# Kernel optimization log

Measured on AMD Instinct MI355X. Metric: run time of the kernel, lower is better.

The kernel has to match this reference:

```python
import jax, jax.numpy as jnp
import numpy as np

DIM = 1024
HID = 2048
E = 8
K = 2
INV_SQRT2 = 1.0 / 1.41421356237


def setup_inputs() -> dict:
    key = jax.random.key(0)
    ks = jax.random.split(key, 10)
    s = lambda fan_in: 1.0 / np.sqrt(fan_in)
    return {
        "x": jax.random.normal(ks[0], (4, 2048, DIM), dtype=jnp.float32),
        "gate_w": jax.random.uniform(ks[1], (DIM, E), jnp.float32, -s(DIM), s(DIM)),
        "gate_b": jnp.zeros((E,), jnp.float32),
        "w1": jax.random.uniform(ks[2], (E, DIM, HID), jnp.float32, -s(DIM), s(DIM)),
        "b1": jnp.zeros((E, HID), jnp.float32),
        "w2": jax.random.uniform(ks[3], (E, DIM, HID), jnp.float32, -s(DIM), s(DIM)),
        "b2": jnp.zeros((E, HID), jnp.float32),
        "w3": jax.random.uniform(ks[4], (E, HID, DIM), jnp.float32, -s(HID), s(HID)),
        "b3": jnp.zeros((E, DIM), jnp.float32),
    }


def reference(x, gate_w, gate_b, w1, b1, w2, b2, w3, b3):
    # Gating
    logits = jnp.einsum("bsd,de->bse", x, gate_w) + gate_b          # [b,s,E]
    scores = jax.nn.softmax(logits, axis=-1)
    topk_scores, topk_idx = jax.lax.top_k(scores, K)                  # [b,s,K]

    # Load-balance (entropy) loss over mean expert usage
    usage = scores.mean(axis=(0, 1))                                   # [E]
    lb_loss = -(usage * jnp.log(usage + 1e-9)).sum()

    # Per-token combine weight for each expert: score if expert in top-k else 0
    onehot = jax.nn.one_hot(topk_idx, E, dtype=x.dtype)               # [b,s,K,E]
    comb = (topk_scores[..., None] * onehot).sum(axis=2)              # [b,s,E]

    # SwiGLU experts (batched over E via einsum)
    h = jnp.einsum("bsd,edh->ebsh", x, w1) + b1[:, None, None, :]
    g = jax.nn.silu(jnp.einsum("bsd,edh->ebsh", x, w2) + b2[:, None, None, :])
    eo = jnp.einsum("ebsh,ehd->ebsd", h * g, w3) + b3[:, None, None, :]
    eo = eo * INV_SQRT2

    # Weighted combine (zero weight where expert not selected)
    out = jnp.einsum("ebsd,bse->bsd", eo, comb)
    return out, lb_loss
```

## Files before the change

kernel.cpp:

```cpp
#include <hip/hip_runtime.h>
#include <cstdio>

#define NTOK 8192
#define DIM 1024
#define HID 2048
#define NE 8
#define NPAIR (NTOK * 2)

typedef __attribute__((ext_vector_type(8))) short bf16x8;
typedef __attribute__((ext_vector_type(4))) float f32x4;

typedef const __attribute__((address_space(1))) void* gas_ptr;
typedef __attribute__((address_space(3))) void* las_ptr;

__device__ __forceinline__ void async16(const void* g, void* s) {
  __builtin_amdgcn_global_load_lds((gas_ptr)g, (las_ptr)s, 16, 0, 0);
}

__device__ __forceinline__ unsigned short f2bf(float f) {
  unsigned int u = __float_as_uint(f);
  u = (u + 0x7fff + ((u >> 16) & 1)) >> 16;
  return (unsigned short)u;
}

__device__ __forceinline__ float bf2f(unsigned short u) {
  return __uint_as_float((unsigned int)u << 16);
}


#define S_BARRIER __builtin_amdgcn_s_barrier()
#define VM_WAIT(N) asm volatile("s_waitcnt vmcnt(" #N ")" ::: "memory")
#define LGKM0 asm volatile("s_waitcnt lgkmcnt(0)" ::: "memory")
#define CFENCE asm volatile("" ::: "memory")

__global__ __launch_bounds__(256) void prepgate_kernel(
    const float* __restrict__ w1, const float* __restrict__ w2,
    const float* __restrict__ w3, unsigned short* __restrict__ w1bt,
    unsigned short* __restrict__ w2bt, unsigned short* __restrict__ w3bt,
    const float* __restrict__ x, const float* __restrict__ gw,
    const float* __restrict__ gb, unsigned short* __restrict__ xb,
    float* __restrict__ scores, int* __restrict__ route_e,
    float* __restrict__ route_w) {
  __shared__ float smem[NE * DIM];
  const int bx = blockIdx.x;
  const int tid = threadIdx.x;

  if (bx < 12288) {
    float (*tT)[65] = reinterpret_cast<float(*)[65]>(smem);
    const int z = bx >> 9;
    const int bxx = bx & 511;
    const int m = z >> 3, e = z & 7;
    int R, C;
    const float* in;
    unsigned short* outp;
    if (m == 0)      { R = DIM; C = HID; in = w1; outp = w1bt; }
    else if (m == 1) { R = DIM; C = HID; in = w2; outp = w2bt; }
    else             { R = HID; C = DIM; in = w3; outp = w3bt; }
    in += (size_t)e * DIM * HID;
    outp += (size_t)e * DIM * HID;

    const int tilesx = C >> 6;
    const int c0 = (bxx % tilesx) * 64;
    const int r0 = (bxx / tilesx) * 64;

    const int cq = tid & 15;
    const int rr = tid >> 4;
#pragma unroll
    for (int p = 0; p < 4; p++) {
      const int r = rr + p * 16;
      const float4 v = *(const float4*)(in + (size_t)(r0 + r) * C + c0 + cq * 4);
      tT[cq * 4 + 0][r] = v.x;
      tT[cq * 4 + 1][r] = v.y;
      tT[cq * 4 + 2][r] = v.z;
      tT[cq * 4 + 3][r] = v.w;
    }
    __syncthreads();
    const int cc8 = tid & 7;
    const int rr2 = tid >> 3;
#pragma unroll
    for (int p = 0; p < 2; p++) {
      const int cc = rr2 + p * 32;
      bf16x8 o;
#pragma unroll
      for (int k = 0; k < 8; k++) o[k] = (short)f2bf(tT[cc][cc8 * 8 + k]);
      *(bf16x8*)(outp + (size_t)(c0 + cc) * R + r0 + cc8 * 8) = o;
    }
    return;
  }

  float (*sgwT)[DIM] = reinterpret_cast<float(*)[DIM]>(smem);
  const int g = bx - 12288;
#pragma unroll
  for (int i = 0; i < 8; i++) {
    const int j = i * 256 + tid;
    const float4 v = ((const float4*)gw)[j];
    const int d = j >> 1, e0 = (j & 1) * 4;
    sgwT[e0 + 0][d] = v.x; sgwT[e0 + 1][d] = v.y;
    sgwT[e0 + 2][d] = v.z; sgwT[e0 + 3][d] = v.w;
  }
  __syncthreads();

  const int wv = tid >> 6, lane = tid & 63;
  const int t = g * 4 + wv;
  float acc[NE] = {0.f, 0.f, 0.f, 0.f, 0.f, 0.f, 0.f, 0.f};
  const float4* x4 = (const float4*)(x + (size_t)t * DIM);
#pragma unroll
  for (int i = 0; i < 4; i++) {
    const float4 xv = x4[i * 64 + lane];
    const int d4 = i * 64 + lane;
    ushort4 xbv;
    xbv.x = f2bf(xv.x); xbv.y = f2bf(xv.y);
    xbv.z = f2bf(xv.z); xbv.w = f2bf(xv.w);
    *(ushort4*)(xb + (size_t)t * DIM + d4 * 4) = xbv;
#pragma unroll
    for (int e = 0; e < NE; e++) {
      const float4 wv4 = *(const float4*)&sgwT[e][d4 * 4];
      acc[e] += xv.x * wv4.x + xv.y * wv4.y + xv.z * wv4.z + xv.w * wv4.w;
    }
  }
#pragma unroll
  for (int e = 0; e < NE; e++)
#pragma unroll
    for (int s = 32; s; s >>= 1) acc[e] += __shfl_xor(acc[e], s, 64);

  if (lane == 0) {
    float l[NE], m = -1e30f;
#pragma unroll
    for (int e = 0; e < NE; e++) { l[e] = acc[e] + gb[e]; m = fmaxf(m, l[e]); }
    float p[NE], sum = 0.f;
#pragma unroll
    for (int e = 0; e < NE; e++) { p[e] = __expf(l[e] - m); sum += p[e]; }
    const float inv = 1.f / sum;
    float s[NE];
#pragma unroll
    for (int e = 0; e < NE; e++) { s[e] = p[e] * inv; scores[t * NE + e] = s[e]; }
    int i1 = 0;
    for (int e = 1; e < NE; e++) if (s[e] > s[i1]) i1 = e;
    int i2 = -1;
    for (int e = 0; e < NE; e++) {
      if (e == i1) continue;
      if (i2 < 0 || s[e] > s[i2]) i2 = e;
    }
    route_e[t * 2] = i1; route_e[t * 2 + 1] = i2;
    route_w[t * 2] = s[i1]; route_w[t * 2 + 1] = s[i2];
  }
}

__global__ void finalize_kernel(const float* __restrict__ scores,
                                const int* __restrict__ route_e,
                                int* __restrict__ ctrl,
                                float* __restrict__ out_lb) {
  __shared__ float red[1024];
  __shared__ int hist[NE];
  const int tid = threadIdx.x;
  if (tid < NE) hist[tid] = 0;
  const int e = tid & 7, row = tid >> 3;
  float s = 0.f;
  for (int i = 0; i < 64; i++) s += scores[(size_t)(row + i * 128) * NE + e];
  red[tid] = s;
  __syncthreads();
#pragma unroll
  for (int i = 0; i < 16; i++)
    atomicAdd(&hist[route_e[i * 1024 + tid]], 1);
  for (int st = 512; st >= 8; st >>= 1) {
    __syncthreads();
    if (tid < st) red[tid] += red[tid + st];
  }
  __syncthreads();
  if (tid == 0) {
    float lb = 0.f;
    for (int ee = 0; ee < NE; ee++) {
      const float u = red[ee] * (1.f / 8192.f);
      lb -= u * __logf(u + 1e-9f);
    }
    *out_lb = lb;
    int o = 0;
    for (int ee = 0; ee < NE; ee++) {
      ctrl[ee] = hist[ee];
      ctrl[8 + ee] = o;
      ctrl[17 + ee] = o;
      o += hist[ee];
    }
    ctrl[16] = o;
  }
}

__global__ __launch_bounds__(256) void scatter_kernel(
    const int* __restrict__ route_e, const float* __restrict__ route_w,
    int* __restrict__ ctrl, int* __restrict__ tok_list,
    float* __restrict__ pair_w, int* __restrict__ pair_pos) {
  __shared__ int lh[NE];
  __shared__ int lbase[NE];
  const int tid = threadIdx.x;
  const int t = blockIdx.x * 256 + tid;
  if (tid < NE) lh[tid] = 0;
  __syncthreads();
  const int e0 = route_e[t * 2], e1 = route_e[t * 2 + 1];
  const int p0 = atomicAdd(&lh[e0], 1);
  const int p1 = atomicAdd(&lh[e1], 1);
  __syncthreads();
  if (tid < NE) lbase[tid] = atomicAdd(&ctrl[17 + tid], lh[tid]);
  __syncthreads();
  const int q0 = lbase[e0] + p0;
  const int q1 = lbase[e1] + p1;
  tok_list[q0] = t;
  pair_w[q0] = route_w[t * 2] * 0.70710678118654752f;
  pair_pos[t * 2] = q0;
  tok_list[q1] = t;
  pair_w[q1] = route_w[t * 2 + 1] * 0.70710678118654752f;
  pair_pos[t * 2 + 1] = q1;
}

__global__ __launch_bounds__(512) void stage1_kernel(
    const unsigned short* __restrict__ xb, const unsigned short* __restrict__ w1bt,
    const unsigned short* __restrict__ w2bt, const float* __restrict__ b1,
    const float* __restrict__ b2, const int* __restrict__ tok_list,
    const int* __restrict__ ctrl, unsigned short* __restrict__ act) {
  const int hbid = blockIdx.x;
  const int xcd = hbid & 7, j = hbid >> 3;
  const int unit = xcd + 8 * (j >> 4);
  const int e = unit >> 5;
  const int ytile = unit & 31;
  const int h0 = (j & 15) * 128;

  const int cnt = ctrl[e];
  if (ytile * 256 >= cnt) return;
  const int off = ctrl[8 + e];
  const int rows = min(256, cnt - ytile * 256);

  __shared__ unsigned short sX[4][256 * 32];
  __shared__ unsigned short sW1[4][128 * 32];
  __shared__ unsigned short sW2[4][128 * 32];

  const int tid = threadIdx.x;
  const int wv = tid >> 6, lane = tid & 63;
  const int cl = ((tid & 3) ^ ((tid >> 3) & 3)) * 8;

  const unsigned short* w1p = w1bt + (size_t)e * HID * DIM + (size_t)h0 * DIM;
  const unsigned short* w2p = w2bt + (size_t)e * HID * DIM + (size_t)h0 * DIM;
  const unsigned short* gx0 =
      xb + (size_t)tok_list[off + ytile * 256 + min(tid >> 2, rows - 1)] * DIM + cl;
  const unsigned short* gx1 =
      xb + (size_t)tok_list[off + ytile * 256 + min(128 + (tid >> 2), rows - 1)] * DIM + cl;
  const unsigned short* gw1 = w1p + (size_t)(tid >> 2) * DIM + cl;
  const unsigned short* gw2 = w2p + (size_t)(tid >> 2) * DIM + cl;

  f32x4 ah[8][2], ag[8][2];
#pragma unroll
  for (int i = 0; i < 8; i++)
#pragma unroll
    for (int j2 = 0; j2 < 2; j2++) {
      ah[i][j2] = (f32x4){0.f, 0.f, 0.f, 0.f};
      ag[i][j2] = (f32x4){0.f, 0.f, 0.f, 0.f};
    }

  const int wr = wv >> 2, wc = wv & 3;
  const int l15 = lane & 15, q = lane >> 4;
  const int pch = (q ^ ((l15 >> 1) & 3)) * 8;

#define S1_STAGE(B)                                   \
  do {                                                \
    async16(gx0, sX[B] + (wv * 64) * 8);              \
    async16(gx1, sX[B] + (512 + wv * 64) * 8);        \
    async16(gw1, sW1[B] + (wv * 64) * 8);             \
    async16(gw2, sW2[B] + (wv * 64) * 8);             \
    gx0 += 32; gx1 += 32; gw1 += 32; gw2 += 32;       \
  } while (0)

  S1_STAGE(0); S1_STAGE(1); S1_STAGE(2);
  VM_WAIT(8);
  S_BARRIER;
  CFENCE;

  const int NT = DIM / 32;
  for (int t = 0; t < NT; t++) {
    const int cur = t & 3;
    bf16x8 bx[8], a1[2], a2[2];
    {
      const unsigned short* xs = sX[cur];
      const unsigned short* w1s = sW1[cur];
      const unsigned short* w2s = sW2[cur];
#pragma unroll
      for (int j2 = 0; j2 < 2; j2++) {
        a1[j2] = *(const bf16x8*)(w1s + (wc * 32 + j2 * 16 + l15) * 32 + pch);
        a2[j2] = *(const bf16x8*)(w2s + (wc * 32 + j2 * 16 + l15) * 32 + pch);
      }
#pragma unroll
      for (int i = 0; i < 8; i++)
        bx[i] = *(const bf16x8*)(xs + (wr * 128 + i * 16 + l15) * 32 + pch);
    }
    if (t < NT - 3) {
      const int nb = (t + 3) & 3;
      S1_STAGE(nb);
    }
    __builtin_amdgcn_s_setprio(1);
#pragma unroll
    for (int i = 0; i < 8; i++) {
      ah[i][0] = __builtin_amdgcn_mfma_f32_16x16x32_bf16(a1[0], bx[i], ah[i][0], 0, 0, 0);
      ag[i][0] = __builtin_amdgcn_mfma_f32_16x16x32_bf16(a2[0], bx[i], ag[i][0], 0, 0, 0);
      ah[i][1] = __builtin_amdgcn_mfma_f32_16x16x32_bf16(a1[1], bx[i], ah[i][1], 0, 0, 0);
      ag[i][1] = __builtin_amdgcn_mfma_f32_16x16x32_bf16(a2[1], bx[i], ag[i][1], 0, 0, 0);
    }
    __builtin_amdgcn_s_setprio(0);
    LGKM0;
    __builtin_amdgcn_sched_barrier(0);
    if (t < NT - 3) VM_WAIT(8);
    else if (t == NT - 3) VM_WAIT(4);
    else if (t == NT - 2) VM_WAIT(0);
    CFENCE;
    S_BARRIER;
  }
#undef S1_STAGE

  f32x4 b1v[2], b2v[2];
#pragma unroll
  for (int j2 = 0; j2 < 2; j2++) {
    const int hc = h0 + wc * 32 + j2 * 16 + q * 4;
    b1v[j2] = *(const f32x4*)(b1 + e * HID + hc);
    b2v[j2] = *(const f32x4*)(b2 + e * HID + hc);
  }
#pragma unroll
  for (int i = 0; i < 8; i++) {
    const int trow = wr * 128 + i * 16 + l15;
    if (trow < rows) {
      const size_t gp = (size_t)(off + ytile * 256 + trow) * HID;
#pragma unroll
      for (int j2 = 0; j2 < 2; j2++) {
        const int hc = h0 + wc * 32 + j2 * 16 + q * 4;
        ushort4 o;
        {
          const float hh = ah[i][j2][0] + b1v[j2][0];
          const float gg = ag[i][j2][0] + b2v[j2][0];
          o.x = f2bf(hh * (gg / (1.f + __expf(-gg))));
        }
        {
          const float hh = ah[i][j2][1] + b1v[j2][1];
          const float gg = ag[i][j2][1] + b2v[j2][1];
          o.y = f2bf(hh * (gg / (1.f + __expf(-gg))));
        }
        {
          const float hh = ah[i][j2][2] + b1v[j2][2];
          const float gg = ag[i][j2][2] + b2v[j2][2];
          o.z = f2bf(hh * (gg / (1.f + __expf(-gg))));
        }
        {
          const float hh = ah[i][j2][3] + b1v[j2][3];
          const float gg = ag[i][j2][3] + b2v[j2][3];
          o.w = f2bf(hh * (gg / (1.f + __expf(-gg))));
        }
        *(ushort4*)(act + gp + hc) = o;
      }
    }
  }
}

__global__ __launch_bounds__(512) void stage2s_kernel(
    const unsigned short* __restrict__ act, const unsigned short* __restrict__ w3bt,
    const float* __restrict__ b3, const float* __restrict__ pair_w,
    const int* __restrict__ ctrl, unsigned short* __restrict__ pair_out) {
  const int hbid = blockIdx.x;
  const int xcd = hbid & 7, j = hbid >> 3;
  const int unit = xcd + 8 * (j >> 2);
  const int e = unit >> 5;
  const int ytile = unit & 31;
  const int d0 = (j & 3) * 256;

  const int cnt = ctrl[e];
  if (ytile * 256 >= cnt) return;
  const int off = ctrl[8 + e];
  const int rows = min(256, cnt - ytile * 256);
  const int rbase = off + ytile * 256;

  __shared__ unsigned short sA[4][256 * 32];
  __shared__ unsigned short sW[4][256 * 32];

  const int tid = threadIdx.x;
  const int wv = tid >> 6, lane = tid & 63;
  const int cl = ((tid & 3) ^ ((tid >> 3) & 3)) * 8;

  const unsigned short* w3p = w3bt + (size_t)e * DIM * HID + (size_t)d0 * HID;
  const unsigned short* ga0 =
      act + (size_t)(rbase + min(tid >> 2, rows - 1)) * HID + cl;
  const unsigned short* ga1 =
      act + (size_t)(rbase + min(128 + (tid >> 2), rows - 1)) * HID + cl;
  const unsigned short* gw0 = w3p + (size_t)(tid >> 2) * HID + cl;
  const unsigned short* gw1 = w3p + (size_t)(128 + (tid >> 2)) * HID + cl;

  f32x4 acc[8][4];
#pragma unroll
  for (int i = 0; i < 8; i++)
#pragma unroll
    for (int jj = 0; jj < 4; jj++) acc[i][jj] = (f32x4){0.f, 0.f, 0.f, 0.f};

  const int wr = wv >> 2, wc = wv & 3;
  const int l15 = lane & 15, q = lane >> 4;
  const int pch = (q ^ ((l15 >> 1) & 3)) * 8;

#define S2_STAGE(B)                                   \
  do {                                                \
    async16(ga0, sA[B] + (wv * 64) * 8);              \
    async16(ga1, sA[B] + (512 + wv * 64) * 8);        \
    async16(gw0, sW[B] + (wv * 64) * 8);              \
    async16(gw1, sW[B] + (512 + wv * 64) * 8);        \
    ga0 += 32; ga1 += 32; gw0 += 32; gw1 += 32;       \
  } while (0)

  S2_STAGE(0); S2_STAGE(1); S2_STAGE(2);
  VM_WAIT(8);
  S_BARRIER;
  CFENCE;

  const int NT = HID / 32;
  for (int t = 0; t < NT; t++) {
    const int cur = t & 3;
    bf16x8 af[8], bf[4];
    {
      const unsigned short* as = sA[cur];
      const unsigned short* ws = sW[cur];
#pragma unroll
      for (int jj = 0; jj < 4; jj++)
        bf[jj] = *(const bf16x8*)(ws + (wc * 64 + jj * 16 + l15) * 32 + pch);
#pragma unroll
      for (int i = 0; i < 8; i++)
        af[i] = *(const bf16x8*)(as + (wr * 128 + i * 16 + l15) * 32 + pch);
    }
    if (t < NT - 3) {
      const int nb = (t + 3) & 3;
      S2_STAGE(nb);
    }
    __builtin_amdgcn_s_setprio(1);
#pragma unroll
    for (int i = 0; i < 8; i++)
#pragma unroll
      for (int jj = 0; jj < 4; jj++)
        acc[i][jj] =
            __builtin_amdgcn_mfma_f32_16x16x32_bf16(af[i], bf[jj], acc[i][jj], 0, 0, 0);
    __builtin_amdgcn_s_setprio(0);
    LGKM0;
    __builtin_amdgcn_sched_barrier(0);
    if (t < NT - 3) VM_WAIT(8);
    else if (t == NT - 3) VM_WAIT(4);
    else if (t == NT - 2) VM_WAIT(0);
    CFENCE;
    S_BARRIER;
  }
#undef S2_STAGE

#pragma unroll
  for (int i = 0; i < 8; i++)
#pragma unroll
    for (int rg = 0; rg < 4; rg++) {
      const int row = wr * 128 + i * 16 + q * 4 + rg;
      if (row < rows) {
        const int pr = rbase + row;
        const float wt = pair_w[pr];
#pragma unroll
        for (int jj = 0; jj < 4; jj++) {
          const int dcol = d0 + wc * 64 + jj * 16 + l15;
          pair_out[(size_t)pr * DIM + dcol] = f2bf((acc[i][jj][rg] + b3[e * DIM + dcol]) * wt);
        }
      }
    }
}

__global__ __launch_bounds__(512) void stage2a_kernel(
    const unsigned short* __restrict__ act, const unsigned short* __restrict__ w3bt,
    const float* __restrict__ b3, const int* __restrict__ tok_list,
    const float* __restrict__ pair_w, const int* __restrict__ ctrl,
    float* __restrict__ out) {
  const int hbid = blockIdx.x;
  const int xcd = hbid & 7, j = hbid >> 3;
  const int unit = xcd + 8 * (j >> 2);
  const int e = unit >> 5;
  const int ytile = unit & 31;
  const int d0 = (j & 3) * 256;

  const int cnt = ctrl[e];
  if (ytile * 256 >= cnt) return;
  const int off = ctrl[8 + e];
  const int rows = min(256, cnt - ytile * 256);
  const int rbase = off + ytile * 256;

  __shared__ unsigned short sA[4][256 * 32];
  __shared__ unsigned short sW[4][256 * 32];

  const int tid = threadIdx.x;
  const int wv = tid >> 6, lane = tid & 63;
  const int cl = ((tid & 3) ^ ((tid >> 3) & 3)) * 8;

  const unsigned short* w3p = w3bt + (size_t)e * DIM * HID + (size_t)d0 * HID;
  const unsigned short* ga0 =
      act + (size_t)(rbase + min(tid >> 2, rows - 1)) * HID + cl;
  const unsigned short* ga1 =
      act + (size_t)(rbase + min(128 + (tid >> 2), rows - 1)) * HID + cl;
  const unsigned short* gw0 = w3p + (size_t)(tid >> 2) * HID + cl;
  const unsigned short* gw1 = w3p + (size_t)(128 + (tid >> 2)) * HID + cl;

  f32x4 acc[8][4];
#pragma unroll
  for (int i = 0; i < 8; i++)
#pragma unroll
    for (int jj = 0; jj < 4; jj++) acc[i][jj] = (f32x4){0.f, 0.f, 0.f, 0.f};

  const int wr = wv >> 2, wc = wv & 3;
  const int l15 = lane & 15, q = lane >> 4;
  const int pch = (q ^ ((l15 >> 1) & 3)) * 8;

#define S2A_STAGE(B)                                  \
  do {                                                \
    async16(ga0, sA[B] + (wv * 64) * 8);              \
    async16(ga1, sA[B] + (512 + wv * 64) * 8);        \
    async16(gw0, sW[B] + (wv * 64) * 8);              \
    async16(gw1, sW[B] + (512 + wv * 64) * 8);        \
    ga0 += 32; ga1 += 32; gw0 += 32; gw1 += 32;       \
  } while (0)

  S2A_STAGE(0); S2A_STAGE(1); S2A_STAGE(2);
  VM_WAIT(8);
  S_BARRIER;
  CFENCE;

  const int NT = HID / 32;
  for (int t = 0; t < NT; t++) {
    const int cur = t & 3;
    bf16x8 af[8], bf[4];
    {
      const unsigned short* as = sA[cur];
      const unsigned short* ws = sW[cur];
#pragma unroll
      for (int jj = 0; jj < 4; jj++)
        bf[jj] = *(const bf16x8*)(ws + (wc * 64 + jj * 16 + l15) * 32 + pch);
#pragma unroll
      for (int i = 0; i < 8; i++)
        af[i] = *(const bf16x8*)(as + (wr * 128 + i * 16 + l15) * 32 + pch);
    }
    if (t < NT - 3) {
      const int nb = (t + 3) & 3;
      S2A_STAGE(nb);
    }
    __builtin_amdgcn_s_setprio(1);
#pragma unroll
    for (int i = 0; i < 8; i++)
#pragma unroll
      for (int jj = 0; jj < 4; jj++)
        acc[i][jj] =
            __builtin_amdgcn_mfma_f32_16x16x32_bf16(af[i], bf[jj], acc[i][jj], 0, 0, 0);
    __builtin_amdgcn_s_setprio(0);
    LGKM0;
    __builtin_amdgcn_sched_barrier(0);
    if (t < NT - 3) VM_WAIT(8);
    else if (t == NT - 3) VM_WAIT(4);
    else if (t == NT - 2) VM_WAIT(0);
    CFENCE;
    S_BARRIER;
  }
#undef S2A_STAGE

#pragma unroll
  for (int i = 0; i < 8; i++)
#pragma unroll
    for (int rg = 0; rg < 4; rg++) {
      const int row = wr * 128 + i * 16 + q * 4 + rg;
      if (row < rows) {
        const int pr = rbase + row;
        const int tok = tok_list[pr];
        const float wt = pair_w[pr];
#pragma unroll
        for (int jj = 0; jj < 4; jj++) {
          const int dcol = d0 + wc * 64 + jj * 16 + l15;
          atomicAdd(out + (size_t)tok * DIM + dcol, (acc[i][jj][rg] + b3[e * DIM + dcol]) * wt);
        }
      }
    }
}

__global__ __launch_bounds__(256) void combine_kernel(
    const unsigned short* __restrict__ pair_out, const int* __restrict__ pair_pos,
    float* __restrict__ out) {
  const int d = threadIdx.x * 4;
#pragma unroll
  for (int tt = 0; tt < 8; tt++) {
    const int t = blockIdx.x * 8 + tt;
    const int p0 = pair_pos[t * 2], p1 = pair_pos[t * 2 + 1];
    const ushort4 a = *(const ushort4*)(pair_out + (size_t)p0 * DIM + d);
    const ushort4 b = *(const ushort4*)(pair_out + (size_t)p1 * DIM + d);
    float4 r;
    r.x = bf2f(a.x) + bf2f(b.x);
    r.y = bf2f(a.y) + bf2f(b.y);
    r.z = bf2f(a.z) + bf2f(b.z);
    r.w = bf2f(a.w) + bf2f(b.w);
    *(float4*)(out + (size_t)t * DIM + d) = r;
  }
}

static const size_t SZ_XB  = (size_t)NTOK * DIM * 2;
static const size_t SZ_W   = (size_t)NE * DIM * HID * 2;
static const size_t SZ_ACT = (size_t)NPAIR * HID * 2;
static const size_t OFF_XB  = 0;
static const size_t OFF_W1  = OFF_XB + SZ_XB;
static const size_t OFF_W2  = OFF_W1 + SZ_W;
static const size_t OFF_W3  = OFF_W2 + SZ_W;
static const size_t OFF_ACT = OFF_W3 + SZ_W;
static const size_t OFF_SC  = OFF_ACT + SZ_ACT;
static const size_t OFF_RE  = OFF_SC + (size_t)NTOK * NE * 4;
static const size_t OFF_RW  = OFF_RE + (size_t)NPAIR * 4;
static const size_t OFF_TL  = OFF_RW + (size_t)NPAIR * 4;
static const size_t OFF_PW  = OFF_TL + (size_t)NPAIR * 4;
static const size_t OFF_PP  = OFF_PW + (size_t)NPAIR * 4;
static const size_t OFF_CT  = OFF_PP + (size_t)NPAIR * 4;
static const size_t WS_BASE = OFF_CT + 128;
static const size_t OFF_PO  = WS_BASE;
static const size_t WS_FULL = OFF_PO + (size_t)NPAIR * DIM * 2;

extern "C" void kernel_launch(void* const* d_in, const int* in_sizes, int n_in,
                              void* d_out, int out_size, void* d_ws, size_t ws_size,
                              hipStream_t stream) {
  const float* x      = (const float*)d_in[0];
  const float* gate_w = (const float*)d_in[1];
  const float* gate_b = (const float*)d_in[2];
  const float* w1     = (const float*)d_in[3];
  const float* b1     = (const float*)d_in[4];
  const float* w2     = (const float*)d_in[5];
  const float* b2     = (const float*)d_in[6];
  const float* w3     = (const float*)d_in[7];
  const float* b3     = (const float*)d_in[8];
  float* out = (float*)d_out;

  if (ws_size < WS_BASE) {
    fprintf(stderr, "kernel_launch: ws_size %zu < needed %zu\n", ws_size, WS_BASE);
    return;
  }
  const bool store_path = (ws_size >= WS_FULL);

  char* ws = (char*)d_ws;
  unsigned short* xb   = (unsigned short*)(ws + OFF_XB);
  unsigned short* w1bt = (unsigned short*)(ws + OFF_W1);
  unsigned short* w2bt = (unsigned short*)(ws + OFF_W2);
  unsigned short* w3bt = (unsigned short*)(ws + OFF_W3);
  unsigned short* act  = (unsigned short*)(ws + OFF_ACT);
  float* scores        = (float*)(ws + OFF_SC);
  int* route_e         = (int*)(ws + OFF_RE);
  float* route_w       = (float*)(ws + OFF_RW);
  int* tok_list        = (int*)(ws + OFF_TL);
  float* pair_w        = (float*)(ws + OFF_PW);
  int* pair_pos        = (int*)(ws + OFF_PP);
  int* ctrl            = (int*)(ws + OFF_CT);
  unsigned short* pout = (unsigned short*)(ws + OFF_PO);

  if (!store_path)
    hipMemsetAsync(d_out, 0, (size_t)out_size * sizeof(float), stream);

  prepgate_kernel<<<14336, 256, 0, stream>>>(w1, w2, w3, w1bt, w2bt, w3bt,
                                             x, gate_w, gate_b, xb, scores,
                                             route_e, route_w);
  finalize_kernel<<<1, 1024, 0, stream>>>(scores, route_e, ctrl, out + (out_size - 1));
  scatter_kernel<<<32, 256, 0, stream>>>(route_e, route_w, ctrl, tok_list, pair_w,
                                         pair_pos);
  stage1_kernel<<<4096, 512, 0, stream>>>(xb, w1bt, w2bt, b1, b2, tok_list, ctrl, act);
  if (store_path) {
    stage2s_kernel<<<1024, 512, 0, stream>>>(act, w3bt, b3, pair_w, ctrl, pout);
    combine_kernel<<<1024, 256, 0, stream>>>(pout, pair_pos, out);
  } else {
    stage2a_kernel<<<1024, 512, 0, stream>>>(act, w3bt, b3, tok_list, pair_w,
                                             ctrl, out);
  }
}
```

Measured before the change: 595.0 us.

## Halve stage-2 output tile width and remap block-to-XCD assignment per expert

Stage-2 GEMM tiles shrink from 256x256 to 256x128 output columns, doubling the grid to 2048 blocks and halving the W3 shared-memory buffer and accumulators. Block IDs in stage 1 and stage 2 are remapped so that each XCD handles a contiguous range of one expert's work, which is meant to improve L2 reuse of expert weights. The smaller tiles should raise occupancy and balance load across CUs when expert token counts vary, but they lower arithmetic intensity because activation tiles are reloaded twice as often.

```diff
diff --git a/kernel.cpp b/kernel.cpp
--- a/kernel.cpp
+++ b/kernel.cpp
@@ -217,11 +217,10 @@
     const float* __restrict__ b2, const int* __restrict__ tok_list,
     const int* __restrict__ ctrl, unsigned short* __restrict__ act) {
   const int hbid = blockIdx.x;
-  const int xcd = hbid & 7, j = hbid >> 3;
-  const int unit = xcd + 8 * (j >> 4);
-  const int e = unit >> 5;
-  const int ytile = unit & 31;
-  const int h0 = (j & 15) * 128;
+  const int lid = ((hbid & 7) << 9) + (hbid >> 3);
+  const int e = lid >> 9;
+  const int ytile = (lid >> 4) & 31;
+  const int h0 = (lid & 15) * 128;
 
   const int cnt = ctrl[e];
   if (ytile * 256 >= cnt) return;
@@ -359,11 +358,10 @@
     const float* __restrict__ b3, const float* __restrict__ pair_w,
     const int* __restrict__ ctrl, unsigned short* __restrict__ pair_out) {
   const int hbid = blockIdx.x;
-  const int xcd = hbid & 7, j = hbid >> 3;
-  const int unit = xcd + 8 * (j >> 2);
-  const int e = unit >> 5;
-  const int ytile = unit & 31;
-  const int d0 = (j & 3) * 256;
+  const int lid = ((hbid & 7) << 8) + (hbid >> 3);
+  const int e = lid >> 8;
+  const int ytile = (lid >> 3) & 31;
+  const int d0 = (lid & 7) * 128;
 
   const int cnt = ctrl[e];
   if (ytile * 256 >= cnt) return;
@@ -372,7 +370,7 @@
   const int rbase = off + ytile * 256;
 
   __shared__ unsigned short sA[4][256 * 32];
-  __shared__ unsigned short sW[4][256 * 32];
+  __shared__ unsigned short sW[4][128 * 32];
 
   const int tid = threadIdx.x;
   const int wv = tid >> 6, lane = tid & 63;
@@ -383,14 +381,13 @@
       act + (size_t)(rbase + min(tid >> 2, rows - 1)) * HID + cl;
   const unsigned short* ga1 =
       act + (size_t)(rbase + min(128 + (tid >> 2), rows - 1)) * HID + cl;
-  const unsigned short* gw0 = w3p + (size_t)(tid >> 2) * HID + cl;
-  const unsigned short* gw1 = w3p + (size_t)(128 + (tid >> 2)) * HID + cl;
-
-  f32x4 acc[8][4];
+  const unsigned short* gw = w3p + (size_t)(tid >> 2) * HID + cl;
+
+  f32x4 acc[8][2];
 #pragma unroll
   for (int i = 0; i < 8; i++)
 #pragma unroll
-    for (int jj = 0; jj < 4; jj++) acc[i][jj] = (f32x4){0.f, 0.f, 0.f, 0.f};
+    for (int jj = 0; jj < 2; jj++) acc[i][jj] = (f32x4){0.f, 0.f, 0.f, 0.f};
 
   const int wr = wv >> 2, wc = wv & 3;
   const int l15 = lane & 15, q = lane >> 4;
@@ -400,26 +397,25 @@
   do {                                                \
     async16(ga0, sA[B] + (wv * 64) * 8);              \
     async16(ga1, sA[B] + (512 + wv * 64) * 8);        \
-    async16(gw0, sW[B] + (wv * 64) * 8);              \
-    async16(gw1, sW[B] + (512 + wv * 64) * 8);        \
-    ga0 += 32; ga1 += 32; gw0 += 32; gw1 += 32;       \
+    async16(gw, sW[B] + (wv * 64) * 8);               \
+    ga0 += 32; ga1 += 32; gw += 32;                   \
   } while (0)
 
   S2_STAGE(0); S2_STAGE(1); S2_STAGE(2);
-  VM_WAIT(8);
+  VM_WAIT(6);
   S_BARRIER;
   CFENCE;
 
   const int NT = HID / 32;
   for (int t = 0; t < NT; t++) {
     const int cur = t & 3;
-    bf16x8 af[8], bf[4];
+    bf16x8 af[8], bf[2];
     {
       const unsigned short* as = sA[cur];
       const unsigned short* ws = sW[cur];
 #pragma unroll
-      for (int jj = 0; jj < 4; jj++)
-        bf[jj] = *(const bf16x8*)(ws + (wc * 64 + jj * 16 + l15) * 32 + pch);
+      for (int jj = 0; jj < 2; jj++)
+        bf[jj] = *(const bf16x8*)(ws + (wc * 32 + jj * 16 + l15) * 32 + pch);
 #pragma unroll
       for (int i = 0; i < 8; i++)
         af[i] = *(const bf16x8*)(as + (wr * 128 + i * 16 + l15) * 32 + pch);
@@ -432,14 +428,14 @@
 #pragma unroll
     for (int i = 0; i < 8; i++)
 #pragma unroll
-      for (int jj = 0; jj < 4; jj++)
+      for (int jj = 0; jj < 2; jj++)
         acc[i][jj] =
             __builtin_amdgcn_mfma_f32_16x16x32_bf16(af[i], bf[jj], acc[i][jj], 0, 0, 0);
     __builtin_amdgcn_s_setprio(0);
     LGKM0;
     __builtin_amdgcn_sched_barrier(0);
-    if (t < NT - 3) VM_WAIT(8);
-    else if (t == NT - 3) VM_WAIT(4);
+    if (t < NT - 3) VM_WAIT(6);
+    else if (t == NT - 3) VM_WAIT(3);
     else if (t == NT - 2) VM_WAIT(0);
     CFENCE;
     S_BARRIER;
@@ -455,8 +451,8 @@
         const int pr = rbase + row;
         const float wt = pair_w[pr];
 #pragma unroll
-        for (int jj = 0; jj < 4; jj++) {
-          const int dcol = d0 + wc * 64 + jj * 16 + l15;
+        for (int jj = 0; jj < 2; jj++) {
+          const int dcol = d0 + wc * 32 + jj * 16 + l15;
           pair_out[(size_t)pr * DIM + dcol] = f2bf((acc[i][jj][rg] + b3[e * DIM + dcol]) * wt);
         }
       }
@@ -469,11 +465,10 @@
     const float* __restrict__ pair_w, const int* __restrict__ ctrl,
     float* __restrict__ out) {
   const int hbid = blockIdx.x;
-  const int xcd = hbid & 7, j = hbid >> 3;
-  const int unit = xcd + 8 * (j >> 2);
-  const int e = unit >> 5;
-  const int ytile = unit & 31;
-  const int d0 = (j & 3) * 256;
+  const int lid = ((hbid & 7) << 8) + (hbid >> 3);
+  const int e = lid >> 8;
+  const int ytile = (lid >> 3) & 31;
+  const int d0 = (lid & 7) * 128;
 
   const int cnt = ctrl[e];
   if (ytile * 256 >= cnt) return;
@@ -482,7 +477,7 @@
   const int rbase = off + ytile * 256;
 
   __shared__ unsigned short sA[4][256 * 32];
-  __shared__ unsigned short sW[4][256 * 32];
+  __shared__ unsigned short sW[4][128 * 32];
 
   const int tid = threadIdx.x;
   const int wv = tid >> 6, lane = tid & 63;
@@ -493,14 +488,13 @@
       act + (size_t)(rbase + min(tid >> 2, rows - 1)) * HID + cl;
   const unsigned short* ga1 =
       act + (size_t)(rbase + min(128 + (tid >> 2), rows - 1)) * HID + cl;
-  const unsigned short* gw0 = w3p + (size_t)(tid >> 2) * HID + cl;
-  const unsigned short* gw1 = w3p + (size_t)(128 + (tid >> 2)) * HID + cl;
-
-  f32x4 acc[8][4];
+  const unsigned short* gw = w3p + (size_t)(tid >> 2) * HID + cl;
+
+  f32x4 acc[8][2];
 #pragma unroll
   for (int i = 0; i < 8; i++)
 #pragma unroll
-    for (int jj = 0; jj < 4; jj++) acc[i][jj] = (f32x4){0.f, 0.f, 0.f, 0.f};
+    for (int jj = 0; jj < 2; jj++) acc[i][jj] = (f32x4){0.f, 0.f, 0.f, 0.f};
 
   const int wr = wv >> 2, wc = wv & 3;
   const int l15 = lane & 15, q = lane >> 4;
@@ -510,26 +504,25 @@
   do {                                                \
     async16(ga0, sA[B] + (wv * 64) * 8);              \
     async16(ga1, sA[B] + (512 + wv * 64) * 8);        \
-    async16(gw0, sW[B] + (wv * 64) * 8);              \
-    async16(gw1, sW[B] + (512 + wv * 64) * 8);        \
-    ga0 += 32; ga1 += 32; gw0 += 32; gw1 += 32;       \
+    async16(gw, sW[B] + (wv * 64) * 8);               \
+    ga0 += 32; ga1 += 32; gw += 32;                   \
   } while (0)
 
   S2A_STAGE(0); S2A_STAGE(1); S2A_STAGE(2);
-  VM_WAIT(8);
+  VM_WAIT(6);
   S_BARRIER;
   CFENCE;
 
   const int NT = HID / 32;
   for (int t = 0; t < NT; t++) {
     const int cur = t & 3;
-    bf16x8 af[8], bf[4];
+    bf16x8 af[8], bf[2];
     {
       const unsigned short* as = sA[cur];
       const unsigned short* ws = sW[cur];
 #pragma unroll
-      for (int jj = 0; jj < 4; jj++)
-        bf[jj] = *(const bf16x8*)(ws + (wc * 64 + jj * 16 + l15) * 32 + pch);
+      for (int jj = 0; jj < 2; jj++)
+        bf[jj] = *(const bf16x8*)(ws + (wc * 32 + jj * 16 + l15) * 32 + pch);
 #pragma unroll
       for (int i = 0; i < 8; i++)
         af[i] = *(const bf16x8*)(as + (wr * 128 + i * 16 + l15) * 32 + pch);
@@ -542,14 +535,14 @@
 #pragma unroll
     for (int i = 0; i < 8; i++)
 #pragma unroll
-      for (int jj = 0; jj < 4; jj++)
+      for (int jj = 0; jj < 2; jj++)
         acc[i][jj] =
             __builtin_amdgcn_mfma_f32_16x16x32_bf16(af[i], bf[jj], acc[i][jj], 0, 0, 0);
     __builtin_amdgcn_s_setprio(0);
     LGKM0;
     __builtin_amdgcn_sched_barrier(0);
-    if (t < NT - 3) VM_WAIT(8);
-    else if (t == NT - 3) VM_WAIT(4);
+    if (t < NT - 3) VM_WAIT(6);
+    else if (t == NT - 3) VM_WAIT(3);
     else if (t == NT - 2) VM_WAIT(0);
     CFENCE;
     S_BARRIER;
@@ -566,8 +559,8 @@
         const int tok = tok_list[pr];
         const float wt = pair_w[pr];
 #pragma unroll
-        for (int jj = 0; jj < 4; jj++) {
-          const int dcol = d0 + wc * 64 + jj * 16 + l15;
+        for (int jj = 0; jj < 2; jj++) {
+          const int dcol = d0 + wc * 32 + jj * 16 + l15;
           atomicAdd(out + (size_t)tok * DIM + dcol, (acc[i][jj][rg] + b3[e * DIM + dcol]) * wt);
         }
       }
@@ -658,10 +651,10 @@
                                          pair_pos);
   stage1_kernel<<<4096, 512, 0, stream>>>(xb, w1bt, w2bt, b1, b2, tok_list, ctrl, act);
   if (store_path) {
-    stage2s_kernel<<<1024, 512, 0, stream>>>(act, w3bt, b3, pair_w, ctrl, pout);
+    stage2s_kernel<<<2048, 512, 0, stream>>>(act, w3bt, b3, pair_w, ctrl, pout);
     combine_kernel<<<1024, 256, 0, stream>>>(pout, pair_pos, out);
   } else {
-    stage2a_kernel<<<1024, 512, 0, stream>>>(act, w3bt, b3, tok_list, pair_w,
+    stage2a_kernel<<<2048, 512, 0, stream>>>(act, w3bt, b3, tok_list, pair_w,
                                              ctrl, out);
   }
 }
```

New measurement: 546.3 us. -8.2%, faster.

## Remap block ids so each XCD owns one expert; one token per combine block

Applied to the files above, without the earlier changes.

Changes the block-index-to-work mapping in the stage1 and stage2 GEMM kernels. Each XCD (selected by hbid&7) now processes all tiles of a single expert, so that expert's weights stay in that XCD's L2 instead of being spread across all XCDs. Before, the eight XCDs shared units interleaved across experts. The combine kernel is also split to one token per block with NTOK blocks, which adds parallelism but raises launch and block-scheduling overhead. Load balance across XCDs now depends on how evenly tokens are routed across experts.

```diff
diff --git a/kernel.cpp b/kernel.cpp
--- a/kernel.cpp
+++ b/kernel.cpp
@@ -217,11 +217,10 @@
     const float* __restrict__ b2, const int* __restrict__ tok_list,
     const int* __restrict__ ctrl, unsigned short* __restrict__ act) {
   const int hbid = blockIdx.x;
-  const int xcd = hbid & 7, j = hbid >> 3;
-  const int unit = xcd + 8 * (j >> 4);
-  const int e = unit >> 5;
-  const int ytile = unit & 31;
-  const int h0 = (j & 15) * 128;
+  const int lid = ((hbid & 7) << 9) + (hbid >> 3);
+  const int e = lid >> 9;
+  const int ytile = (lid >> 4) & 31;
+  const int h0 = (lid & 15) * 128;
 
   const int cnt = ctrl[e];
   if (ytile * 256 >= cnt) return;
@@ -359,11 +358,10 @@
     const float* __restrict__ b3, const float* __restrict__ pair_w,
     const int* __restrict__ ctrl, unsigned short* __restrict__ pair_out) {
   const int hbid = blockIdx.x;
-  const int xcd = hbid & 7, j = hbid >> 3;
-  const int unit = xcd + 8 * (j >> 2);
-  const int e = unit >> 5;
-  const int ytile = unit & 31;
-  const int d0 = (j & 3) * 256;
+  const int lid = ((hbid & 7) << 7) + (hbid >> 3);
+  const int e = lid >> 7;
+  const int ytile = (lid >> 2) & 31;
+  const int d0 = (lid & 3) * 256;
 
   const int cnt = ctrl[e];
   if (ytile * 256 >= cnt) return;
@@ -469,11 +467,10 @@
     const float* __restrict__ pair_w, const int* __restrict__ ctrl,
     float* __restrict__ out) {
   const int hbid = blockIdx.x;
-  const int xcd = hbid & 7, j = hbid >> 3;
-  const int unit = xcd + 8 * (j >> 2);
-  const int e = unit >> 5;
-  const int ytile = unit & 31;
-  const int d0 = (j & 3) * 256;
+  const int lid = ((hbid & 7) << 7) + (hbid >> 3);
+  const int e = lid >> 7;
+  const int ytile = (lid >> 2) & 31;
+  const int d0 = (lid & 3) * 256;
 
   const int cnt = ctrl[e];
   if (ytile * 256 >= cnt) return;
@@ -577,20 +574,17 @@
 __global__ __launch_bounds__(256) void combine_kernel(
     const unsigned short* __restrict__ pair_out, const int* __restrict__ pair_pos,
     float* __restrict__ out) {
+  const int t = blockIdx.x;
   const int d = threadIdx.x * 4;
-#pragma unroll
-  for (int tt = 0; tt < 8; tt++) {
-    const int t = blockIdx.x * 8 + tt;
-    const int p0 = pair_pos[t * 2], p1 = pair_pos[t * 2 + 1];
-    const ushort4 a = *(const ushort4*)(pair_out + (size_t)p0 * DIM + d);
-    const ushort4 b = *(const ushort4*)(pair_out + (size_t)p1 * DIM + d);
-    float4 r;
-    r.x = bf2f(a.x) + bf2f(b.x);
-    r.y = bf2f(a.y) + bf2f(b.y);
-    r.z = bf2f(a.z) + bf2f(b.z);
-    r.w = bf2f(a.w) + bf2f(b.w);
-    *(float4*)(out + (size_t)t * DIM + d) = r;
-  }
+  const int p0 = pair_pos[t * 2], p1 = pair_pos[t * 2 + 1];
+  const ushort4 a = *(const ushort4*)(pair_out + (size_t)p0 * DIM + d);
+  const ushort4 b = *(const ushort4*)(pair_out + (size_t)p1 * DIM + d);
+  float4 r;
+  r.x = bf2f(a.x) + bf2f(b.x);
+  r.y = bf2f(a.y) + bf2f(b.y);
+  r.z = bf2f(a.z) + bf2f(b.z);
+  r.w = bf2f(a.w) + bf2f(b.w);
+  *(float4*)(out + (size_t)t * DIM + d) = r;
 }
 
 static const size_t SZ_XB  = (size_t)NTOK * DIM * 2;
@@ -659,7 +653,7 @@
   stage1_kernel<<<4096, 512, 0, stream>>>(xb, w1bt, w2bt, b1, b2, tok_list, ctrl, act);
   if (store_path) {
     stage2s_kernel<<<1024, 512, 0, stream>>>(act, w3bt, b3, pair_w, ctrl, pout);
-    combine_kernel<<<1024, 256, 0, stream>>>(pout, pair_pos, out);
+    combine_kernel<<<NTOK, 256, 0, stream>>>(pout, pair_pos, out);
   } else {
     stage2a_kernel<<<1024, 512, 0, stream>>>(act, w3bt, b3, tok_list, pair_w,
                                              ctrl, out);
```

Measured after the change: 542.9 us. 8.8% less time.
